# Performance work log

Measured on AMD Instinct MI355X. Metric: run time of the kernel, lower is better.

Reference implementation:

```python
import jax, jax.numpy as jnp
import numpy as np

N = 8192
D_IN = 512
D_OUT = 128
N_EDGES = 131072
ALPHA = 0.01


def setup_inputs() -> dict:
    key = jax.random.key(0)
    ks = jax.random.split(key, 6)
    x = jax.random.normal(ks[0], (N, D_IN), dtype=jnp.float32)
    edge_index = jax.random.randint(ks[1], (2, N_EDGES), 0, N, dtype=jnp.int64)
    W1 = jax.random.normal(ks[2], (D_IN, D_OUT), dtype=jnp.float32) * (1.0 / np.sqrt(D_IN))
    b1 = jnp.zeros((D_OUT,), dtype=jnp.float32)
    W2 = jax.random.normal(ks[3], (D_IN, D_OUT), dtype=jnp.float32) * (1.0 / np.sqrt(D_IN))
    b2 = jnp.zeros((D_OUT,), dtype=jnp.float32)
    return {"x": x, "edge_index": edge_index, "W1": W1, "b1": b1, "W2": W2, "b2": b2}


def gcn_sparse(x, W, b, src, dst, n):
    # PyG GCNConv: add self loops (weight 1), symmetric D^-1/2 (A+I) D^-1/2 normalization,
    # deg computed over target index, messages src -> dst.
    h = x @ W  # [n, d_out]
    deg = jnp.zeros((n,), dtype=x.dtype).at[dst].add(1.0) + 1.0  # +1 for self loop
    dinv = jnp.where(deg > 0, 1.0 / jnp.sqrt(deg), 0.0)
    norm = dinv[src] * dinv[dst]  # [E]
    out = jnp.zeros_like(h).at[dst].add(norm[:, None] * h[src])
    out = out + (dinv * dinv)[:, None] * h  # self-loop messages
    return out + b


def gcn_dense_2hop(x, W, b, src, dst, n):
    # Mirrors high_adj: sparse A (ones, duplicates summed), A @ A, dense nonzero -> binary
    # 2-hop edges; then GCNConv on that graph (self loops appended on top of existing diag).
    A = jnp.zeros((n, n), dtype=x.dtype).at[src, dst].add(1.0)
    A2 = (A @ A > 0).astype(x.dtype)  # binary 2-hop adjacency [n, n]
    idx = jnp.arange(n)
    A2hat = A2.at[idx, idx].add(1.0)  # add_self_loops appends weight-1 self loops
    deg = A2hat.sum(axis=0)  # deg over target (column) index
    dinv = jnp.where(deg > 0, 1.0 / jnp.sqrt(deg), 0.0)
    h = x @ W
    # out[i] = dinv[i] * sum_j A2hat[j, i] * dinv[j] * h[j]
    out = dinv[:, None] * (A2hat.T @ (dinv[:, None] * h))
    return out + b


def reference(x, edge_index, W1, b1, W2, b2):
    src, dst = edge_index[0], edge_index[1]
    n = x.shape[0]
    x1 = gcn_sparse(x, W1, b1, src, dst, n)
    x2 = gcn_dense_2hop(x, W2, b2, src, dst, n)
    return jnp.concatenate([(1.0 - ALPHA) * x1, ALPHA * x2], axis=1)
```

## Files before the change

kernel.cpp:

```cpp
#include <hip/hip_runtime.h>
#include <hip/hip_bf16.h>


#define NN   8192
#define NE   131072
#define DIN  512
#define DO   128

using u64 = unsigned long long;
typedef __attribute__((ext_vector_type(8))) short short8v;
typedef __attribute__((ext_vector_type(4))) float f32x4;

static constexpr size_t OFF_G1   = 0;
static constexpr size_t OFF_G2B  = OFF_G1   + 4194304;
static constexpr size_t OFF_AT   = OFF_G2B  + 2097152;
static constexpr size_t OFF_A2T  = OFF_AT   + 8388608;
static constexpr size_t OFF_XH   = OFF_A2T  + 8388608;
static constexpr size_t OFF_XL   = OFF_XH   + 8388608;
static constexpr size_t OFF_BT   = OFF_XL   + 8388608;
static constexpr size_t OFF_CNT  = OFF_BT   + 786432;
static constexpr size_t OFF_FILL = OFF_CNT  + 32768;
static constexpr size_t OFF_RP   = OFF_FILL + 32768;
static constexpr size_t OFF_CSR  = OFF_RP   + 33024;
static constexpr size_t OFF_DI1  = OFF_CSR  + 524288;
static constexpr size_t OFF_DI2  = OFF_DI1  + 32768;

__device__ __forceinline__ unsigned short f2bf(float f) {
  unsigned u = __float_as_uint(f);
  return (unsigned short)((u + 0x7fffu + ((u >> 16) & 1u)) >> 16);
}
__device__ __forceinline__ float bf2f(unsigned short h) {
  return __uint_as_float((unsigned)h << 16);
}
__device__ __forceinline__ void load_lds16(const void* g, void* l) {
  __builtin_amdgcn_global_load_lds((const __attribute__((address_space(1))) void*)g,
                                   (__attribute__((address_space(3))) void*)l, 16, 0, 0);
}


__global__ void k_zero(u64* __restrict__ AT,
                       unsigned* __restrict__ cnt, unsigned* __restrict__ fill) {
  size_t tid = (size_t)blockIdx.x * blockDim.x + threadIdx.x;
  size_t stride = (size_t)gridDim.x * blockDim.x;
  for (size_t i = tid; i < (size_t)NN * 128; i += stride) AT[i] = 0ull;
  if (tid < NN) { cnt[tid] = 0u; fill[tid] = 0u; }
}

__global__ void k_hist(const int* __restrict__ ei, unsigned* __restrict__ cnt) {
  int e = blockIdx.x * blockDim.x + threadIdx.x;
  if (e >= NE) return;
  atomicAdd(&cnt[ei[NE + e]], 1u);
}

__global__ __launch_bounds__(1024) void k_scan(const unsigned* __restrict__ cnt,
                                               unsigned* __restrict__ row_ptr,
                                               float* __restrict__ dinv1) {
  __shared__ unsigned sums[1024];
  int t = threadIdx.x;
  unsigned v[8];
  unsigned s = 0;
  #pragma unroll
  for (int i = 0; i < 8; i++) { v[i] = cnt[t * 8 + i]; s += v[i]; }
  sums[t] = s;
  __syncthreads();
  for (int off = 1; off < 1024; off *= 2) {
    unsigned add = (t >= off) ? sums[t - off] : 0u;
    __syncthreads();
    sums[t] += add;
    __syncthreads();
  }
  unsigned base = (t == 0) ? 0u : sums[t - 1];
  #pragma unroll
  for (int i = 0; i < 8; i++) {
    row_ptr[t * 8 + i] = base;
    base += v[i];
    dinv1[t * 8 + i] = rsqrtf((float)v[i] + 1.0f);
  }
  if (t == 1023) row_ptr[NN] = base;
}

__global__ void k_scatter(const int* __restrict__ ei, const unsigned* __restrict__ row_ptr,
                          unsigned* __restrict__ fill, unsigned* __restrict__ csr_src,
                          u64* __restrict__ AT) {
  int e = blockIdx.x * blockDim.x + threadIdx.x;
  if (e >= NE) return;
  int s = ei[e];
  int d = ei[NE + e];
  unsigned pos = atomicAdd(&fill[d], 1u);
  csr_src[row_ptr[d] + pos] = (unsigned)s;
  atomicOr(&AT[(size_t)d * 128 + (s >> 6)], 1ull << (s & 63));
}

__global__ __launch_bounds__(512) void k_a2t(const u64* __restrict__ AT,
                                             u64* __restrict__ A2T,
                                             float* __restrict__ dinv2) {
  const int i = blockIdx.x, t = threadIdx.x;
  __shared__ unsigned pc[128];
  __shared__ unsigned short list[512];
  __shared__ u64 redB[4][128];
  u64 w0 = 0ull;
  if (t < 128) {
    w0 = AT[(size_t)i * 128 + t];
    pc[t] = (unsigned)__popcll(w0);
  }
  __syncthreads();
  for (int off = 1; off < 128; off <<= 1) {
    unsigned add = (t >= off && t < 128) ? pc[t - off] : 0u;
    __syncthreads();
    if (t < 128) pc[t] += add;
    __syncthreads();
  }
  if (t < 128) {
    unsigned base = (t == 0) ? 0u : pc[t - 1];
    u64 m = w0;
    while (m) {
      int b = __ffsll(m) - 1;
      m &= m - 1;
      list[base++] = (unsigned short)(t * 64 + b);
    }
  }
  __syncthreads();
  const unsigned total = pc[127];
  const int q = t >> 7, c = t & 127;
  u64 acc = 0ull;
  #pragma unroll 4
  for (unsigned k = q; k < total; k += 4)
    acc |= AT[(size_t)list[k] * 128 + c];
  redB[q][c] = acc;
  __syncthreads();
  if (t < 128) {
    u64 u = redB[0][t] | redB[1][t] | redB[2][t] | redB[3][t];
    A2T[(size_t)i * 128 + t] = u;
    pc[t] = (unsigned)__popcll(u);
  }
  __syncthreads();
  for (int s = 64; s > 0; s >>= 1) {
    if (t < s) pc[t] += pc[t + s];
    __syncthreads();
  }
  if (t == 0) dinv2[i] = rsqrtf((float)pc[0] + 1.0f);
}

__global__ void k_conv(const float* __restrict__ x, unsigned short* __restrict__ xh,
                       unsigned short* __restrict__ xl) {
  size_t i = (size_t)blockIdx.x * blockDim.x + threadIdx.x;
  size_t stride = (size_t)gridDim.x * blockDim.x;
  for (size_t p = i; p < (size_t)NN * DIN / 4; p += stride) {
    float4 v = ((const float4*)x)[p];
    ushort4 h, l;
    h.x = f2bf(v.x); l.x = f2bf(v.x - bf2f(h.x));
    h.y = f2bf(v.y); l.y = f2bf(v.y - bf2f(h.y));
    h.z = f2bf(v.z); l.z = f2bf(v.z - bf2f(h.z));
    h.w = f2bf(v.w); l.w = f2bf(v.w - bf2f(h.w));
    ((ushort4*)xh)[p] = h;
    ((ushort4*)xl)[p] = l;
  }
}

__global__ __launch_bounds__(256) void k_bprep(const float* __restrict__ W1,
                                               const float* __restrict__ W2,
                                               unsigned short* __restrict__ Bt) {
  const int t = blockIdx.x * 256 + threadIdx.x;
  if (t >= 8192) return;
  const int n = t & 127, kb = (t >> 7) << 3;
  short8v vh, vl, v2;
  #pragma unroll
  for (int j = 0; j < 8; j++) {
    float w = W1[(size_t)(kb + j) * DO + n];
    unsigned short h = f2bf(w);
    vh[j] = (short)h;
    vl[j] = (short)f2bf(w - bf2f(h));
    v2[j] = (short)f2bf(W2[(size_t)(kb + j) * DO + n]);
  }
  unsigned short* r1 = &Bt[(size_t)n * 1536];
  *(short8v*)&r1[kb]        = vh;
  *(short8v*)&r1[512 + kb]  = vl;
  *(short8v*)&r1[1024 + kb] = vh;
  *(short8v*)&Bt[(size_t)(128 + n) * 1536 + kb] = v2;
}

__global__ __launch_bounds__(256) void k_gemm(const unsigned short* __restrict__ xh,
                                              const unsigned short* __restrict__ xl,
                                              const unsigned short* __restrict__ Bt,
                                              const float* __restrict__ dinv1,
                                              const float* __restrict__ dinv2,
                                              float* __restrict__ g1,
                                              unsigned short* __restrict__ g2b) {
  const int bm = blockIdx.x, bn = blockIdx.y;
  const int Kext = (bn < 2) ? 1536 : 512;
  __shared__ __align__(16) unsigned short As[4096];
  __shared__ __align__(16) unsigned short Bs[4096];
  const int tid = threadIdx.x;
  const int lane = tid & 63, wv = tid >> 6;
  const int wr = wv >> 1, wc = wv & 1;

  const int c0 = tid, c1 = tid + 256;
  const int cb0 = c0 >> 6, l0 = c0 & 63;
  const int cb1 = c1 >> 6, l1 = c1 & 63;
  const int rT0 = (cb0 >> 1) * 16 + (l0 & 15), kc0 = (cb0 & 1) * 4 + (l0 >> 4);
  const int rT1 = (cb1 >> 1) * 16 + (l1 & 15), kc1 = (cb1 & 1) * 4 + (l1 >> 4);
  const size_t gA0 = (size_t)(bm * 64 + rT0) * DIN + kc0 * 8;
  const size_t gA1 = (size_t)(bm * 64 + rT1) * DIN + kc1 * 8;
  const size_t gB0 = (size_t)(bn * 64 + rT0) * 1536 + kc0 * 8;
  const size_t gB1 = (size_t)(bn * 64 + rT1) * 1536 + kc1 * 8;

  const int lofs = lane * 8;

  f32x4 acc00 = {0.f, 0.f, 0.f, 0.f};
  f32x4 acc01 = acc00, acc10 = acc00, acc11 = acc00;

  for (int k0 = 0; k0 < Kext; k0 += 64) {
    const unsigned short* sA =
        (k0 < 512) ? (xh + k0) : (k0 < 1024) ? (xh + (k0 - 512)) : (xl + (k0 - 1024));
    load_lds16(sA + gA0, &As[c0 * 8]);
    load_lds16(sA + gA1, &As[c1 * 8]);
    load_lds16(Bt + k0 + gB0, &Bs[c0 * 8]);
    load_lds16(Bt + k0 + gB1, &Bs[c1 * 8]);
    __syncthreads();
    #pragma unroll
    for (int ks = 0; ks < 2; ks++) {
      short8v a0 = *(const short8v*)&As[(wr * 4 + ks) * 512 + lofs];
      short8v a1 = *(const short8v*)&As[(wr * 4 + 2 + ks) * 512 + lofs];
      short8v b0 = *(const short8v*)&Bs[(wc * 4 + ks) * 512 + lofs];
      short8v b1 = *(const short8v*)&Bs[(wc * 4 + 2 + ks) * 512 + lofs];
      acc00 = __builtin_amdgcn_mfma_f32_16x16x32_bf16(a0, b0, acc00, 0, 0, 0);
      acc01 = __builtin_amdgcn_mfma_f32_16x16x32_bf16(a0, b1, acc01, 0, 0, 0);
      acc10 = __builtin_amdgcn_mfma_f32_16x16x32_bf16(a1, b0, acc10, 0, 0, 0);
      acc11 = __builtin_amdgcn_mfma_f32_16x16x32_bf16(a1, b1, acc11, 0, 0, 0);
    }
    __syncthreads();
  }

  const int colb = lane & 15;
  const int rowb = (lane >> 4) << 2;
  #pragma unroll
  for (int m = 0; m < 2; m++) {
    #pragma unroll
    for (int n = 0; n < 2; n++) {
      f32x4 a = (m == 0) ? (n == 0 ? acc00 : acc01) : (n == 0 ? acc10 : acc11);
      const int cl = wc * 32 + n * 16 + colb;
      #pragma unroll
      for (int r = 0; r < 4; r++) {
        const int gr = bm * 64 + wr * 32 + m * 16 + rowb + r;
        if (bn < 2) {
          const int gc = bn * 64 + cl;
          g1[(size_t)gr * DO + gc] = dinv1[gr] * a[r];
        } else {
          const int gc = (bn - 2) * 64 + cl;
          g2b[(size_t)gr * DO + gc] = f2bf(dinv2[gr] * a[r]);
        }
      }
    }
  }
}

__global__ __launch_bounds__(512) void k_spmm1(const float* __restrict__ g1,
                                               const unsigned* __restrict__ row_ptr,
                                               const unsigned* __restrict__ csr_src,
                                               const float* __restrict__ dinv1,
                                               const float* __restrict__ b1,
                                               float* __restrict__ out) {
  const int i = blockIdx.x, t = threadIdx.x;
  __shared__ float redA[8][128];
  const int q = t >> 6, c = t & 63;
  const unsigned lo = row_ptr[i], hi = row_ptr[i + 1];
  float a0 = 0.f, a1 = 0.f;
  #pragma unroll 2
  for (unsigned e = lo + q; e < hi; e += 8) {
    unsigned j = csr_src[e];
    float2 v = *(const float2*)&g1[(size_t)j * DO + 2 * c];
    a0 += v.x; a1 += v.y;
  }
  redA[q][2 * c] = a0;
  redA[q][2 * c + 1] = a1;
  __syncthreads();
  if (t < 128) {
    float s = g1[(size_t)i * DO + t];
    #pragma unroll
    for (int r = 0; r < 8; r++) s += redA[r][t];
    out[(size_t)i * 256 + t] = 0.99f * (dinv1[i] * s + b1[t]);
  }
}

__global__ __launch_bounds__(512) void k_spmm2(const unsigned short* __restrict__ g2b,
                                               const u64* __restrict__ A2T,
                                               const float* __restrict__ dinv2,
                                               const float* __restrict__ b2,
                                               float* __restrict__ out) {
  const int i = blockIdx.x, t = threadIdx.x;
  __shared__ unsigned pc[128];
  __shared__ unsigned short list[8192];
  __shared__ float redA[8][128];
  u64 w0 = 0ull;
  if (t < 128) {
    w0 = A2T[(size_t)i * 128 + t];
    pc[t] = (unsigned)__popcll(w0);
  }
  __syncthreads();
  for (int off = 1; off < 128; off <<= 1) {
    unsigned add = (t >= off && t < 128) ? pc[t - off] : 0u;
    __syncthreads();
    if (t < 128) pc[t] += add;
    __syncthreads();
  }
  if (t < 128) {
    unsigned base = (t == 0) ? 0u : pc[t - 1];
    u64 m = w0;
    while (m) {
      int b = __ffsll(m) - 1;
      m &= m - 1;
      list[base++] = (unsigned short)(t * 64 + b);
    }
  }
  __syncthreads();
  const unsigned total = pc[127];
  const int q = t >> 6, c = t & 63;
  float a0 = 0.f, a1 = 0.f;
  #pragma unroll 4
  for (unsigned k = q; k < total; k += 8) {
    unsigned j = list[k];
    unsigned u = *(const unsigned*)&g2b[(size_t)j * DO + 2 * c];
    a0 += __uint_as_float(u << 16);
    a1 += __uint_as_float(u & 0xffff0000u);
  }
  redA[q][2 * c] = a0;
  redA[q][2 * c + 1] = a1;
  __syncthreads();
  if (t < 128) {
    float s = bf2f(g2b[(size_t)i * DO + t]);
    #pragma unroll
    for (int r = 0; r < 8; r++) s += redA[r][t];
    out[(size_t)i * 256 + 128 + t] = 0.01f * (dinv2[i] * s + b2[t]);
  }
}


extern "C" void kernel_launch(void* const* d_in, const int* in_sizes, int n_in,
                              void* d_out, int out_size, void* d_ws, size_t ws_size,
                              hipStream_t stream) {
  const float* x  = (const float*)d_in[0];
  const int*   ei = (const int*)d_in[1];
  const float* W1 = (const float*)d_in[2];
  const float* b1 = (const float*)d_in[3];
  const float* W2 = (const float*)d_in[4];
  const float* b2 = (const float*)d_in[5];
  float* out = (float*)d_out;
  char* ws = (char*)d_ws;

  float* g1              = (float*)(ws + OFF_G1);
  unsigned short* g2b    = (unsigned short*)(ws + OFF_G2B);
  u64* AT                = (u64*)(ws + OFF_AT);
  u64* A2T               = (u64*)(ws + OFF_A2T);
  unsigned short* xh     = (unsigned short*)(ws + OFF_XH);
  unsigned short* xl     = (unsigned short*)(ws + OFF_XL);
  unsigned short* Bt     = (unsigned short*)(ws + OFF_BT);
  unsigned* cnt          = (unsigned*)(ws + OFF_CNT);
  unsigned* fill         = (unsigned*)(ws + OFF_FILL);
  unsigned* row_ptr      = (unsigned*)(ws + OFF_RP);
  unsigned* csr_src      = (unsigned*)(ws + OFF_CSR);
  float* dinv1           = (float*)(ws + OFF_DI1);
  float* dinv2           = (float*)(ws + OFF_DI2);

  k_zero<<<1024, 256, 0, stream>>>(AT, cnt, fill);
  k_hist<<<NE / 256, 256, 0, stream>>>(ei, cnt);
  k_scan<<<1, 1024, 0, stream>>>(cnt, row_ptr, dinv1);
  k_scatter<<<NE / 256, 256, 0, stream>>>(ei, row_ptr, fill, csr_src, AT);
  k_a2t<<<NN, 512, 0, stream>>>(AT, A2T, dinv2);
  k_conv<<<2048, 256, 0, stream>>>(x, xh, xl);
  k_bprep<<<32, 256, 0, stream>>>(W1, W2, Bt);
  dim3 gg(NN / 64, 4);
  k_gemm<<<gg, 256, 0, stream>>>(xh, xl, Bt, dinv1, dinv2, g1, g2b);
  k_spmm1<<<NN, 512, 0, stream>>>(g1, row_ptr, csr_src, dinv1, b1, out);
  k_spmm2<<<NN, 512, 0, stream>>>(g2b, A2T, dinv2, b2, out);
}
```

Before: 218.5 us.

## Fuse prep kernels and merge both SpMM passes into one 256-thread kernel

Combines the x bf16 split conversion and the weight packing into one launch, with blocks partitioned by block index. Merges the 1-hop CSR aggregation and the 2-hop bitmask aggregation into a single per-row kernel with 256 threads instead of two 512-thread kernels. The 2-hop gather now reads four bf16 values per thread (uint2) so fewer threads cover the 128 columns. This removes two kernel launches and shares the block's setup work, but each block now runs both aggregations one after the other with half the threads, which may lower memory-level parallelism per row.

```diff
diff --git a/kernel.cpp b/kernel.cpp
--- a/kernel.cpp
+++ b/kernel.cpp
@@ -141,42 +141,43 @@
   if (t == 0) dinv2[i] = rsqrtf((float)pc[0] + 1.0f);
 }
 
-__global__ void k_conv(const float* __restrict__ x, unsigned short* __restrict__ xh,
-                       unsigned short* __restrict__ xl) {
-  size_t i = (size_t)blockIdx.x * blockDim.x + threadIdx.x;
-  size_t stride = (size_t)gridDim.x * blockDim.x;
-  for (size_t p = i; p < (size_t)NN * DIN / 4; p += stride) {
-    float4 v = ((const float4*)x)[p];
-    ushort4 h, l;
-    h.x = f2bf(v.x); l.x = f2bf(v.x - bf2f(h.x));
-    h.y = f2bf(v.y); l.y = f2bf(v.y - bf2f(h.y));
-    h.z = f2bf(v.z); l.z = f2bf(v.z - bf2f(h.z));
-    h.w = f2bf(v.w); l.w = f2bf(v.w - bf2f(h.w));
-    ((ushort4*)xh)[p] = h;
-    ((ushort4*)xl)[p] = l;
-  }
-}
-
-__global__ __launch_bounds__(256) void k_bprep(const float* __restrict__ W1,
-                                               const float* __restrict__ W2,
-                                               unsigned short* __restrict__ Bt) {
-  const int t = blockIdx.x * 256 + threadIdx.x;
-  if (t >= 8192) return;
-  const int n = t & 127, kb = (t >> 7) << 3;
-  short8v vh, vl, v2;
-  #pragma unroll
-  for (int j = 0; j < 8; j++) {
-    float w = W1[(size_t)(kb + j) * DO + n];
-    unsigned short h = f2bf(w);
-    vh[j] = (short)h;
-    vl[j] = (short)f2bf(w - bf2f(h));
-    v2[j] = (short)f2bf(W2[(size_t)(kb + j) * DO + n]);
-  }
-  unsigned short* r1 = &Bt[(size_t)n * 1536];
-  *(short8v*)&r1[kb]        = vh;
-  *(short8v*)&r1[512 + kb]  = vl;
-  *(short8v*)&r1[1024 + kb] = vh;
-  *(short8v*)&Bt[(size_t)(128 + n) * 1536 + kb] = v2;
+__global__ __launch_bounds__(256) void k_prep(const float* __restrict__ x,
+                                              const float* __restrict__ W1,
+                                              const float* __restrict__ W2,
+                                              unsigned short* __restrict__ xh,
+                                              unsigned short* __restrict__ xl,
+                                              unsigned short* __restrict__ Bt) {
+  if (blockIdx.x < 2048) {
+    size_t i = (size_t)blockIdx.x * 256 + threadIdx.x;
+    size_t stride = (size_t)2048 * 256;
+    for (size_t p = i; p < (size_t)NN * DIN / 4; p += stride) {
+      float4 v = ((const float4*)x)[p];
+      ushort4 h, l;
+      h.x = f2bf(v.x); l.x = f2bf(v.x - bf2f(h.x));
+      h.y = f2bf(v.y); l.y = f2bf(v.y - bf2f(h.y));
+      h.z = f2bf(v.z); l.z = f2bf(v.z - bf2f(h.z));
+      h.w = f2bf(v.w); l.w = f2bf(v.w - bf2f(h.w));
+      ((ushort4*)xh)[p] = h;
+      ((ushort4*)xl)[p] = l;
+    }
+  } else {
+    const int t = (blockIdx.x - 2048) * 256 + threadIdx.x;
+    const int n = t & 127, kb = (t >> 7) << 3;
+    short8v vh, vl, v2;
+    #pragma unroll
+    for (int j = 0; j < 8; j++) {
+      float w = W1[(size_t)(kb + j) * DO + n];
+      unsigned short h = f2bf(w);
+      vh[j] = (short)h;
+      vl[j] = (short)f2bf(w - bf2f(h));
+      v2[j] = (short)f2bf(W2[(size_t)(kb + j) * DO + n]);
+    }
+    unsigned short* r1 = &Bt[(size_t)n * 1536];
+    *(short8v*)&r1[kb]        = vh;
+    *(short8v*)&r1[512 + kb]  = vl;
+    *(short8v*)&r1[1024 + kb] = vh;
+    *(short8v*)&Bt[(size_t)(128 + n) * 1536 + kb] = v2;
+  }
 }
 
 __global__ __launch_bounds__(256) void k_gemm(const unsigned short* __restrict__ xh,
@@ -254,43 +255,42 @@
   }
 }
 
-__global__ __launch_bounds__(512) void k_spmm1(const float* __restrict__ g1,
-                                               const unsigned* __restrict__ row_ptr,
-                                               const unsigned* __restrict__ csr_src,
-                                               const float* __restrict__ dinv1,
-                                               const float* __restrict__ b1,
-                                               float* __restrict__ out) {
-  const int i = blockIdx.x, t = threadIdx.x;
-  __shared__ float redA[8][128];
-  const int q = t >> 6, c = t & 63;
-  const unsigned lo = row_ptr[i], hi = row_ptr[i + 1];
-  float a0 = 0.f, a1 = 0.f;
-  #pragma unroll 2
-  for (unsigned e = lo + q; e < hi; e += 8) {
-    unsigned j = csr_src[e];
-    float2 v = *(const float2*)&g1[(size_t)j * DO + 2 * c];
-    a0 += v.x; a1 += v.y;
-  }
-  redA[q][2 * c] = a0;
-  redA[q][2 * c + 1] = a1;
-  __syncthreads();
-  if (t < 128) {
-    float s = g1[(size_t)i * DO + t];
-    #pragma unroll
-    for (int r = 0; r < 8; r++) s += redA[r][t];
-    out[(size_t)i * 256 + t] = 0.99f * (dinv1[i] * s + b1[t]);
-  }
-}
-
-__global__ __launch_bounds__(512) void k_spmm2(const unsigned short* __restrict__ g2b,
-                                               const u64* __restrict__ A2T,
-                                               const float* __restrict__ dinv2,
-                                               const float* __restrict__ b2,
-                                               float* __restrict__ out) {
+__global__ __launch_bounds__(256) void k_spmm(const float* __restrict__ g1,
+                                              const unsigned* __restrict__ row_ptr,
+                                              const unsigned* __restrict__ csr_src,
+                                              const float* __restrict__ dinv1,
+                                              const float* __restrict__ b1,
+                                              const unsigned short* __restrict__ g2b,
+                                              const u64* __restrict__ A2T,
+                                              const float* __restrict__ dinv2,
+                                              const float* __restrict__ b2,
+                                              float* __restrict__ out) {
   const int i = blockIdx.x, t = threadIdx.x;
   __shared__ unsigned pc[128];
   __shared__ unsigned short list[8192];
   __shared__ float redA[8][128];
+
+  {
+    const int q = t >> 6, c = t & 63;
+    const unsigned lo = row_ptr[i], hi = row_ptr[i + 1];
+    float a0 = 0.f, a1 = 0.f;
+    #pragma unroll 4
+    for (unsigned e = lo + q; e < hi; e += 4) {
+      unsigned j = csr_src[e];
+      float2 v = *(const float2*)&g1[(size_t)j * DO + 2 * c];
+      a0 += v.x; a1 += v.y;
+    }
+    redA[q][2 * c] = a0;
+    redA[q][2 * c + 1] = a1;
+    __syncthreads();
+    if (t < 128) {
+      float s = g1[(size_t)i * DO + t]
+              + redA[0][t] + redA[1][t] + redA[2][t] + redA[3][t];
+      out[(size_t)i * 256 + t] = 0.99f * (dinv1[i] * s + b1[t]);
+    }
+  }
+  __syncthreads();
+
   u64 w0 = 0ull;
   if (t < 128) {
     w0 = A2T[(size_t)i * 128 + t];
@@ -314,17 +314,21 @@
   }
   __syncthreads();
   const unsigned total = pc[127];
-  const int q = t >> 6, c = t & 63;
-  float a0 = 0.f, a1 = 0.f;
+  const int q = t >> 5, c = t & 31;
+  float a0 = 0.f, a1 = 0.f, a2 = 0.f, a3 = 0.f;
   #pragma unroll 4
   for (unsigned k = q; k < total; k += 8) {
     unsigned j = list[k];
-    unsigned u = *(const unsigned*)&g2b[(size_t)j * DO + 2 * c];
-    a0 += __uint_as_float(u << 16);
-    a1 += __uint_as_float(u & 0xffff0000u);
-  }
-  redA[q][2 * c] = a0;
-  redA[q][2 * c + 1] = a1;
+    uint2 u = *(const uint2*)&g2b[(size_t)j * DO + 4 * c];
+    a0 += __uint_as_float(u.x << 16);
+    a1 += __uint_as_float(u.x & 0xffff0000u);
+    a2 += __uint_as_float(u.y << 16);
+    a3 += __uint_as_float(u.y & 0xffff0000u);
+  }
+  redA[q][4 * c]     = a0;
+  redA[q][4 * c + 1] = a1;
+  redA[q][4 * c + 2] = a2;
+  redA[q][4 * c + 3] = a3;
   __syncthreads();
   if (t < 128) {
     float s = bf2f(g2b[(size_t)i * DO + t]);
@@ -366,10 +370,9 @@
   k_scan<<<1, 1024, 0, stream>>>(cnt, row_ptr, dinv1);
   k_scatter<<<NE / 256, 256, 0, stream>>>(ei, row_ptr, fill, csr_src, AT);
   k_a2t<<<NN, 512, 0, stream>>>(AT, A2T, dinv2);
-  k_conv<<<2048, 256, 0, stream>>>(x, xh, xl);
-  k_bprep<<<32, 256, 0, stream>>>(W1, W2, Bt);
+  k_prep<<<2080, 256, 0, stream>>>(x, W1, W2, xh, xl, Bt);
   dim3 gg(NN / 64, 4);
   k_gemm<<<gg, 256, 0, stream>>>(xh, xl, Bt, dinv1, dinv2, g1, g2b);
-  k_spmm1<<<NN, 512, 0, stream>>>(g1, row_ptr, csr_src, dinv1, b1, out);
-  k_spmm2<<<NN, 512, 0, stream>>>(g2b, A2T, dinv2, b2, out);
-}
+  k_spmm<<<NN, 256, 0, stream>>>(g1, row_ptr, csr_src, dinv1, b1,
+                                 g2b, A2T, dinv2, b2, out);
+}
```

Result: faster. 207.5 us (-5.0%).
